# Kernel optimization log

Hardware: AMD Instinct MI355X
Metric: run time of the kernel (lower is better)

## Reference

```python
import jax, jax.numpy as jnp
import numpy as np

B, T, H = 4, 2048, 1024
NH = 16
HD = H // NH  # 64
NEG_INF = -1.0e9  # module uses -1e9, not -inf


def setup_inputs() -> dict:
    key = jax.random.key(0)
    k1, k2, k3 = jax.random.split(key, 3)
    x = jax.random.normal(k1, (B, T, H), dtype=jnp.float32)
    W_qkv = jax.random.normal(k2, (3 * H, H), dtype=jnp.float32) * (1.0 / np.sqrt(H))
    W_out = jax.random.normal(k3, (H, H), dtype=jnp.float32) * (1.0 / np.sqrt(H))
    return {"x": x, "W_qkv": W_qkv, "W_out": W_out}


def reference(x, W_qkv, W_out):
    Bx, Tx, C = x.shape
    qkv = x @ W_qkv.T                              # [B,T,3H]
    q, k, v = jnp.split(qkv, 3, axis=-1)
    # [B,T,H] -> [B,NH,T,HD]
    q = q.reshape(Bx, Tx, NH, HD).transpose(0, 2, 1, 3)
    k = k.reshape(Bx, Tx, NH, HD).transpose(0, 2, 1, 3)
    v = v.reshape(Bx, Tx, NH, HD).transpose(0, 2, 1, 3)
    scale = 1.0 / np.sqrt(HD)
    scores = jnp.einsum('bhqd,bhkd->bhqk', q, k) * scale  # [B,NH,T,T]
    causal = jnp.tril(jnp.ones((Tx, Tx), dtype=bool))[None, None]
    scores = jnp.where(causal, scores, jnp.asarray(NEG_INF, scores.dtype))
    attn = jax.nn.softmax(scores, axis=-1)
    out = jnp.einsum('bhqk,bhkd->bhqd', attn, v)   # [B,NH,T,HD]
    out = out.transpose(0, 2, 1, 3).reshape(Bx, Tx, C)
    return out @ W_out.T
```

## Files before the change

### kernel.cpp

```cpp
#include <hip/hip_runtime.h>
#include <hip/hip_bf16.h>


typedef unsigned short ushort_t;
typedef __attribute__((ext_vector_type(8))) short  s8v;
typedef __attribute__((ext_vector_type(4))) float  f4v;
typedef __attribute__((ext_vector_type(4))) unsigned int u4v;

__device__ inline ushort_t f2bf(float f) {
    unsigned u = __builtin_bit_cast(unsigned, f);
    u += 0x7fffu + ((u >> 16) & 1u);
    return (ushort_t)(u >> 16);
}

__device__ inline void gload16(const ushort_t* g, ushort_t* l) {
    __builtin_amdgcn_global_load_lds(
        (const __attribute__((address_space(1))) unsigned int*)g,
        (__attribute__((address_space(3))) unsigned int*)l, 16, 0, 0);
}

__global__ __launch_bounds__(256) void cast_all(
    const float* __restrict__ x, const float* __restrict__ wqkv,
    const float* __restrict__ wout, ushort_t* __restrict__ xb,
    ushort_t* __restrict__ wqkvb, ushort_t* __restrict__ woutb)
{
    int i = blockIdx.x * 256 + threadIdx.x;
    const float* src; ushort_t* dst; int off;
    if (i < 1048576)      { src = x;    dst = xb;    off = i; }
    else if (i < 1441792) { src = wqkv; dst = wqkvb; off = i - 1048576; }
    else                  { src = wout; dst = woutb; off = i - 1441792; }
    const float* p = src + (size_t)off * 8;
    f4v a = *(const f4v*)p;
    f4v b = *(const f4v*)(p + 4);
    union { u4v v; ushort_t u[8]; } o;
    #pragma unroll
    for (int j = 0; j < 4; j++) { o.u[j] = f2bf(a[j]); o.u[j + 4] = f2bf(b[j]); }
    *(u4v*)(dst + (size_t)off * 8) = o.v;
}

template<int MODE>
__global__ __launch_bounds__(256) void gemm_nt(
    const ushort_t* __restrict__ A, const ushort_t* __restrict__ Bm,
    ushort_t* __restrict__ o0, ushort_t* __restrict__ o1, ushort_t* __restrict__ o2,
    float* __restrict__ of)
{
    __shared__ __align__(16) ushort_t SH[32768];

    const int tid  = threadIdx.x;
    const int m0   = blockIdx.x * 128;
    const int n0   = blockIdx.y * 128;
    const int wave = tid >> 6, lane = tid & 63;
    const int wr = wave >> 1, wc = wave & 1;
    const int lhi = lane >> 4, llo = lane & 15;
    const int sgch = ((lane & 7) ^ (lane >> 3)) * 8;

    auto stage = [&](int k0, int buf) {
        #pragma unroll
        for (int p = 0; p < 4; p++) {
            int row = wave * 32 + p * 8 + (lane >> 3);
            gload16(A  + (size_t)(m0 + row) * 1024 + k0 + sgch,
                    &SH[buf * 8192 + row * 64 + (lane & 7) * 8]);
            gload16(Bm + (size_t)(n0 + row) * 1024 + k0 + sgch,
                    &SH[16384 + buf * 8192 + row * 64 + (lane & 7) * 8]);
        }
    };

    f4v acc[4][4] = {};
    int buf = 0;
    const int xs = llo & 7;

    stage(0, 0);
    __syncthreads();

    for (int k0 = 0; k0 < 1024; k0 += 64) {
        if (k0 + 64 < 1024) stage(k0 + 64, buf ^ 1);

        #pragma unroll
        for (int s = 0; s < 2; s++) {
            s8v a[4], b[4];
            #pragma unroll
            for (int i = 0; i < 4; i++)
                a[i] = *(const s8v*)&SH[buf * 8192
                        + (wr * 64 + i * 16 + llo) * 64 + ((s * 4 + lhi) ^ xs) * 8];
            #pragma unroll
            for (int i = 0; i < 4; i++)
                b[i] = *(const s8v*)&SH[16384 + buf * 8192
                        + (wc * 64 + i * 16 + llo) * 64 + ((s * 4 + lhi) ^ xs) * 8];
            #pragma unroll
            for (int i = 0; i < 4; i++)
                #pragma unroll
                for (int j = 0; j < 4; j++)
                    acc[i][j] = __builtin_amdgcn_mfma_f32_16x16x32_bf16(a[i], b[j], acc[i][j], 0, 0, 0);
        }

        __syncthreads();
        buf ^= 1;
    }

    if (MODE == 0 && n0 >= 2048) {
        const int hbase = (n0 - 2048) >> 6;
        const int t0b   = m0 & 2047;
        const int bb    = m0 >> 11;
        #pragma unroll 1
        for (int p = 0; p < 2; p++) {
            __syncthreads();
            if (wr == p) {
                #pragma unroll
                for (int i = 0; i < 4; i++)
                    #pragma unroll
                    for (int j = 0; j < 4; j++) {
                        union { unsigned long long q; ushort_t u[4]; } w;
                        #pragma unroll
                        for (int r = 0; r < 4; r++) w.u[r] = f2bf(acc[i][j][r]);
                        int nrel = wc * 64 + j * 16 + llo;
                        *(unsigned long long*)&SH[nrel * 68 + i * 16 + lhi * 4] = w.q;
                    }
            }
            __syncthreads();
            #pragma unroll
            for (int cc = 0; cc < 4; cc++) {
                int c  = cc * 256 + tid;
                int nn = c >> 3, sp0 = (c & 7) * 8;
                union { s8v v; ushort_t u[8]; } o;
                #pragma unroll
                for (int i2 = 0; i2 < 8; i2++) {
                    int sp = sp0 + i2;
                    int k  = ((sp >> 5) << 5) | ((sp & 1) << 4) | ((sp & 31) >> 1);
                    o.u[i2] = SH[nn * 68 + k];
                }
                int head = hbase + (nn >> 6), d = nn & 63;
                size_t bh = (size_t)(bb * 16 + head);
                *(s8v*)(o2 + ((bh * 64 + d) * 2048 + t0b + p * 64 + sp0)) = o.v;
            }
        }
        return;
    }

    #pragma unroll
    for (int i = 0; i < 4; i++) {
        #pragma unroll
        for (int j = 0; j < 4; j++) {
            #pragma unroll
            for (int r = 0; r < 4; r++) {
                int m = m0 + wr * 64 + i * 16 + lhi * 4 + r;
                int n = n0 + wc * 64 + j * 16 + llo;
                if (MODE == 1) {
                    of[(size_t)m * 1024 + n] = acc[i][j][r];
                } else {
                    float val = acc[i][j][r];
                    int b  = m >> 11, t = m & 2047;
                    int which = n >> 10, hh = n & 1023;
                    int head = hh >> 6, d = hh & 63;
                    size_t bh = (size_t)(b * 16 + head);
                    if (which == 0)
                        o0[(size_t)m * 1024 + hh] = f2bf(val * 0.18033688011112042f);
                    else
                        o1[(bh * 2048 + t) * 64 + d] = f2bf(val);
                }
            }
        }
    }
}

__global__ __launch_bounds__(512, 4) void attn_kernel(
    const ushort_t* __restrict__ q_ws, const ushort_t* __restrict__ k_ws,
    const ushort_t* __restrict__ v_ws, ushort_t* __restrict__ ao_ws)
{
    const int bh   = blockIdx.y;
    const int p    = (bh < 32) ? blockIdx.x : 7 - blockIdx.x;
    const int tid  = threadIdx.x;
    const int wave = tid >> 6, lane = tid & 63;
    const int lhi = lane >> 4, llo = lane & 15;
    const int b = bh >> 4, head = bh & 15;

    const ushort_t* Kb = k_ws + (size_t)bh * 2048 * 64;
    const ushort_t* Vb = v_ws + (size_t)bh * 64 * 2048;

    __shared__ __align__(16) ushort_t Ks [2][4096];
    __shared__ __align__(16) ushort_t Vts[2][4096];
    __shared__ __align__(16) ushort_t Ps [8][2][1280];

    const int srow = wave * 8 + (lane >> 3);
    const int gch  = ((lane & 7) ^ (srow & 7)) * 8;
    auto stage = [&](int t, int buf) {
        const int kk0 = t * 64;
        gload16(Kb + (size_t)(kk0 + srow) * 64 + gch,
                &Ks[buf][srow * 64 + (lane & 7) * 8]);
        gload16(Vb + (size_t)srow * 2048 + kk0 + gch,
                &Vts[buf][srow * 64 + (lane & 7) * 8]);
    };

    const int qt  = (wave >> 2) ? (15 - p) : p;
    const int wq0 = qt * 128 + (wave & 3) * 32;

    s8v qf[2][2];
    #pragma unroll
    for (int g = 0; g < 2; g++) {
        const ushort_t* Qp = q_ws + (size_t)(b * 2048 + wq0 + g * 16 + llo) * 1024 + head * 64;
        qf[g][0] = *(const s8v*)(Qp + lhi * 8);
        qf[g][1] = *(const s8v*)(Qp + 32 + lhi * 8);
    }

    f4v o[2][4] = {};
    float lsum[2][4] = {};

    const int ntb = 32 - 2 * p;
    const int xs  = llo & 7;
    int cur = 0;

    stage(0, 0);
    __syncthreads();

    #pragma unroll 1
    for (int t = 0; t < ntb; t++) {
        if (t + 1 < ntb) stage(t + 1, cur ^ 1);

        const int kk0 = t * 64;
        if (kk0 <= wq0 + 31) {
            f4v s0[4], s1[4];
            __builtin_amdgcn_s_setprio(1);
            #pragma unroll
            for (int c = 0; c < 4; c++) {
                const int rb = (c * 16 + llo) * 64;
                s8v kb0 = *(const s8v*)&Ks[cur][rb + ((lhi    ) ^ xs) * 8];
                s8v kb1 = *(const s8v*)&Ks[cur][rb + ((4 + lhi) ^ xs) * 8];
                f4v z0 = {}, z1 = {};
                z0 = __builtin_amdgcn_mfma_f32_16x16x32_bf16(qf[0][0], kb0, z0, 0, 0, 0);
                z0 = __builtin_amdgcn_mfma_f32_16x16x32_bf16(qf[0][1], kb1, z0, 0, 0, 0);
                z1 = __builtin_amdgcn_mfma_f32_16x16x32_bf16(qf[1][0], kb0, z1, 0, 0, 0);
                z1 = __builtin_amdgcn_mfma_f32_16x16x32_bf16(qf[1][1], kb1, z1, 0, 0, 0);
                s0[c] = z0; s1[c] = z1;
            }
            __builtin_amdgcn_s_setprio(0);

            #pragma unroll
            for (int g = 0; g < 2; g++) {
                const int qrb = wq0 + g * 16;
                f4v* s = g ? s1 : s0;
                if ((kk0 + 63) > qrb) {
                    #pragma unroll
                    for (int c = 0; c < 4; c++) {
                        int kkg = kk0 + c * 16 + llo;
                        #pragma unroll
                        for (int r = 0; r < 4; r++)
                            if (kkg > qrb + lhi * 4 + r) s[c][r] = -1e9f;
                    }
                }
                #pragma unroll
                for (int h = 0; h < 2; h++) {
                    #pragma unroll
                    for (int r = 0; r < 4; r++) {
                        float p0 = __builtin_amdgcn_exp2f(s[2 * h][r]);
                        float p1 = __builtin_amdgcn_exp2f(s[2 * h + 1][r]);
                        lsum[g][r] += p0 + p1;
                        unsigned pk;
                        asm("v_cvt_pk_bf16_f32 %0, %1, %2" : "=v"(pk) : "v"(p0), "v"(p1));
                        *(unsigned*)&Ps[wave][g][h * 640 + (lhi * 4 + r) * 40 + llo * 2] = pk;
                    }
                }
            }

            s8v pa[2][2];
            #pragma unroll
            for (int g = 0; g < 2; g++) {
                pa[g][0] = *(const s8v*)&Ps[wave][g][llo * 40 + lhi * 8];
                pa[g][1] = *(const s8v*)&Ps[wave][g][640 + llo * 40 + lhi * 8];
            }
            __builtin_amdgcn_s_setprio(1);
            #pragma unroll
            for (int cd = 0; cd < 4; cd++) {
                const int rb = (cd * 16 + llo) * 64;
                s8v vb0 = *(const s8v*)&Vts[cur][rb + ((lhi    ) ^ xs) * 8];
                s8v vb1 = *(const s8v*)&Vts[cur][rb + ((4 + lhi) ^ xs) * 8];
                #pragma unroll
                for (int g = 0; g < 2; g++) {
                    o[g][cd] = __builtin_amdgcn_mfma_f32_16x16x32_bf16(pa[g][0], vb0, o[g][cd], 0, 0, 0);
                    o[g][cd] = __builtin_amdgcn_mfma_f32_16x16x32_bf16(pa[g][1], vb1, o[g][cd], 0, 0, 0);
                }
            }
            __builtin_amdgcn_s_setprio(0);
        }

        __syncthreads();
        cur ^= 1;
    }

    #pragma unroll
    for (int off = 1; off < 16; off <<= 1)
        #pragma unroll
        for (int g = 0; g < 2; g++)
            #pragma unroll
            for (int r = 0; r < 4; r++)
                lsum[g][r] += __shfl_xor(lsum[g][r], off, 64);

    #pragma unroll
    for (int g = 0; g < 2; g++)
        #pragma unroll
        for (int cd = 0; cd < 4; cd++)
            #pragma unroll
            for (int r = 0; r < 4; r++) {
                int qq = wq0 + g * 16 + lhi * 4 + r;
                int d  = cd * 16 + llo;
                ao_ws[((size_t)(b * 2048 + qq)) * 1024 + head * 64 + d] =
                    f2bf(o[g][cd][r] / lsum[g][r]);
            }
}

extern "C" void kernel_launch(void* const* d_in, const int* in_sizes, int n_in,
                              void* d_out, int out_size, void* d_ws, size_t ws_size,
                              hipStream_t stream) {
    const float* x    = (const float*)d_in[0];
    const float* wqkv = (const float*)d_in[1];
    const float* wout = (const float*)d_in[2];

    ushort_t* wqkvb = (ushort_t*)d_ws;
    ushort_t* woutb = wqkvb + 3145728;
    ushort_t* xb    = woutb + 1048576;
    ushort_t* q_ws  = xb + 8388608;
    ushort_t* k_ws  = q_ws + 8388608;
    ushort_t* v_ws  = k_ws + 8388608;
    ushort_t* ao_ws = xb;
    float*    out   = (float*)d_out;

    cast_all<<<6144, 256, 0, stream>>>(x, wqkv, wout, xb, wqkvb, woutb);
    gemm_nt<0><<<dim3(64, 24), 256, 0, stream>>>(xb, wqkvb, q_ws, k_ws, v_ws, nullptr);
    attn_kernel<<<dim3(8, 64), 512, 0, stream>>>(q_ws, k_ws, v_ws, ao_ws);
    gemm_nt<1><<<dim3(64, 8), 256, 0, stream>>>(ao_ws, woutb, nullptr, nullptr, nullptr, out);
}
```

Before: 225.5 us.

## Give each attention wave 64 query rows with 4 waves per block

Attention blocks shrink from 8 waves to 4, and each wave now covers 64 query rows (four 16-row groups) instead of 32. K and V fragments loaded from LDS are reused across four MFMA row groups, which cuts LDS reads per unit of compute. Diagonal masking now applies only to the single tile where the key block equals the wave's query start, and each wave loads two staging chunks per tile. The cost is more accumulator registers and lower occupancy (launch bound of 256 threads, 2 blocks per CU), so there is less latency hiding.

```diff
diff --git a/kernel.cpp b/kernel.cpp
--- a/kernel.cpp
+++ b/kernel.cpp
@@ -162,7 +162,7 @@
     }
 }
 
-__global__ __launch_bounds__(512, 4) void attn_kernel(
+__global__ __launch_bounds__(256, 2) void attn_kernel(
     const ushort_t* __restrict__ q_ws, const ushort_t* __restrict__ k_ws,
     const ushort_t* __restrict__ v_ws, ushort_t* __restrict__ ao_ws)
 {
@@ -178,31 +178,34 @@
 
     __shared__ __align__(16) ushort_t Ks [2][4096];
     __shared__ __align__(16) ushort_t Vts[2][4096];
-    __shared__ __align__(16) ushort_t Ps [8][2][1280];
-
-    const int srow = wave * 8 + (lane >> 3);
-    const int gch  = ((lane & 7) ^ (srow & 7)) * 8;
+    __shared__ __align__(16) ushort_t Ps [4][4][1280];
+
+    const int gch = ((lane & 7) ^ (lane >> 3)) * 8;
     auto stage = [&](int t, int buf) {
         const int kk0 = t * 64;
-        gload16(Kb + (size_t)(kk0 + srow) * 64 + gch,
-                &Ks[buf][srow * 64 + (lane & 7) * 8]);
-        gload16(Vb + (size_t)srow * 2048 + kk0 + gch,
-                &Vts[buf][srow * 64 + (lane & 7) * 8]);
+        #pragma unroll
+        for (int i = 0; i < 2; i++) {
+            int row = wave * 8 + 32 * i + (lane >> 3);
+            gload16(Kb + (size_t)(kk0 + row) * 64 + gch,
+                    &Ks[buf][(wave * 64 + 256 * i + lane) * 8]);
+            gload16(Vb + (size_t)row * 2048 + kk0 + gch,
+                    &Vts[buf][(wave * 64 + 256 * i + lane) * 8]);
+        }
     };
 
-    const int qt  = (wave >> 2) ? (15 - p) : p;
-    const int wq0 = qt * 128 + (wave & 3) * 32;
-
-    s8v qf[2][2];
-    #pragma unroll
-    for (int g = 0; g < 2; g++) {
+    const int qt  = (wave >> 1) ? (15 - p) : p;
+    const int wq0 = qt * 128 + (wave & 1) * 64;
+
+    s8v qf[4][2];
+    #pragma unroll
+    for (int g = 0; g < 4; g++) {
         const ushort_t* Qp = q_ws + (size_t)(b * 2048 + wq0 + g * 16 + llo) * 1024 + head * 64;
         qf[g][0] = *(const s8v*)(Qp + lhi * 8);
         qf[g][1] = *(const s8v*)(Qp + 32 + lhi * 8);
     }
 
-    f4v o[2][4] = {};
-    float lsum[2][4] = {};
+    f4v o[4][4] = {};
+    float lsum[4][4] = {};
 
     const int ntb = 32 - 2 * p;
     const int xs  = llo & 7;
@@ -216,28 +219,31 @@
         if (t + 1 < ntb) stage(t + 1, cur ^ 1);
 
         const int kk0 = t * 64;
-        if (kk0 <= wq0 + 31) {
-            f4v s0[4], s1[4];
-            __builtin_amdgcn_s_setprio(1);
+        if (kk0 <= wq0) {
+            const bool dm = (kk0 == wq0);
+
+            s8v kb[4][2];
             #pragma unroll
             for (int c = 0; c < 4; c++) {
                 const int rb = (c * 16 + llo) * 64;
-                s8v kb0 = *(const s8v*)&Ks[cur][rb + ((lhi    ) ^ xs) * 8];
-                s8v kb1 = *(const s8v*)&Ks[cur][rb + ((4 + lhi) ^ xs) * 8];
-                f4v z0 = {}, z1 = {};
-                z0 = __builtin_amdgcn_mfma_f32_16x16x32_bf16(qf[0][0], kb0, z0, 0, 0, 0);
-                z0 = __builtin_amdgcn_mfma_f32_16x16x32_bf16(qf[0][1], kb1, z0, 0, 0, 0);
-                z1 = __builtin_amdgcn_mfma_f32_16x16x32_bf16(qf[1][0], kb0, z1, 0, 0, 0);
-                z1 = __builtin_amdgcn_mfma_f32_16x16x32_bf16(qf[1][1], kb1, z1, 0, 0, 0);
-                s0[c] = z0; s1[c] = z1;
-            }
-            __builtin_amdgcn_s_setprio(0);
-
-            #pragma unroll
-            for (int g = 0; g < 2; g++) {
+                kb[c][0] = *(const s8v*)&Ks[cur][rb + ((lhi    ) ^ xs) * 8];
+                kb[c][1] = *(const s8v*)&Ks[cur][rb + ((4 + lhi) ^ xs) * 8];
+            }
+
+            #pragma unroll
+            for (int g = 0; g < 4; g++) {
                 const int qrb = wq0 + g * 16;
-                f4v* s = g ? s1 : s0;
-                if ((kk0 + 63) > qrb) {
+                f4v s[4];
+                __builtin_amdgcn_s_setprio(1);
+                #pragma unroll
+                for (int c = 0; c < 4; c++) {
+                    f4v z = {};
+                    z = __builtin_amdgcn_mfma_f32_16x16x32_bf16(qf[g][0], kb[c][0], z, 0, 0, 0);
+                    z = __builtin_amdgcn_mfma_f32_16x16x32_bf16(qf[g][1], kb[c][1], z, 0, 0, 0);
+                    s[c] = z;
+                }
+                __builtin_amdgcn_s_setprio(0);
+                if (dm) {
                     #pragma unroll
                     for (int c = 0; c < 4; c++) {
                         int kkg = kk0 + c * 16 + llo;
@@ -260,25 +266,25 @@
                 }
             }
 
-            s8v pa[2][2];
-            #pragma unroll
-            for (int g = 0; g < 2; g++) {
-                pa[g][0] = *(const s8v*)&Ps[wave][g][llo * 40 + lhi * 8];
-                pa[g][1] = *(const s8v*)&Ps[wave][g][640 + llo * 40 + lhi * 8];
-            }
-            __builtin_amdgcn_s_setprio(1);
+            s8v vb[4][2];
             #pragma unroll
             for (int cd = 0; cd < 4; cd++) {
                 const int rb = (cd * 16 + llo) * 64;
-                s8v vb0 = *(const s8v*)&Vts[cur][rb + ((lhi    ) ^ xs) * 8];
-                s8v vb1 = *(const s8v*)&Vts[cur][rb + ((4 + lhi) ^ xs) * 8];
-                #pragma unroll
-                for (int g = 0; g < 2; g++) {
-                    o[g][cd] = __builtin_amdgcn_mfma_f32_16x16x32_bf16(pa[g][0], vb0, o[g][cd], 0, 0, 0);
-                    o[g][cd] = __builtin_amdgcn_mfma_f32_16x16x32_bf16(pa[g][1], vb1, o[g][cd], 0, 0, 0);
-                }
-            }
-            __builtin_amdgcn_s_setprio(0);
+                vb[cd][0] = *(const s8v*)&Vts[cur][rb + ((lhi    ) ^ xs) * 8];
+                vb[cd][1] = *(const s8v*)&Vts[cur][rb + ((4 + lhi) ^ xs) * 8];
+            }
+            #pragma unroll
+            for (int g = 0; g < 4; g++) {
+                s8v pa0 = *(const s8v*)&Ps[wave][g][llo * 40 + lhi * 8];
+                s8v pa1 = *(const s8v*)&Ps[wave][g][640 + llo * 40 + lhi * 8];
+                __builtin_amdgcn_s_setprio(1);
+                #pragma unroll
+                for (int cd = 0; cd < 4; cd++) {
+                    o[g][cd] = __builtin_amdgcn_mfma_f32_16x16x32_bf16(pa0, vb[cd][0], o[g][cd], 0, 0, 0);
+                    o[g][cd] = __builtin_amdgcn_mfma_f32_16x16x32_bf16(pa1, vb[cd][1], o[g][cd], 0, 0, 0);
+                }
+                __builtin_amdgcn_s_setprio(0);
+            }
         }
 
         __syncthreads();
@@ -288,13 +294,13 @@
     #pragma unroll
     for (int off = 1; off < 16; off <<= 1)
         #pragma unroll
-        for (int g = 0; g < 2; g++)
+        for (int g = 0; g < 4; g++)
             #pragma unroll
             for (int r = 0; r < 4; r++)
                 lsum[g][r] += __shfl_xor(lsum[g][r], off, 64);
 
     #pragma unroll
-    for (int g = 0; g < 2; g++)
+    for (int g = 0; g < 4; g++)
         #pragma unroll
         for (int cd = 0; cd < 4; cd++)
             #pragma unroll
@@ -324,6 +330,6 @@
 
     cast_all<<<6144, 256, 0, stream>>>(x, wqkv, wout, xb, wqkvb, woutb);
     gemm_nt<0><<<dim3(64, 24), 256, 0, stream>>>(xb, wqkvb, q_ws, k_ws, v_ws, nullptr);
-    attn_kernel<<<dim3(8, 64), 512, 0, stream>>>(q_ws, k_ws, v_ws, ao_ws);
+    attn_kernel<<<dim3(8, 64), 256, 0, stream>>>(q_ws, k_ws, v_ws, ao_ws);
     gemm_nt<1><<<dim3(64, 8), 256, 0, stream>>>(ao_ws, woutb, nullptr, nullptr, nullptr, out);
 }
```

New measurement: 243.3 us. +7.9%, slower.

## Split attention work across 16 waves with 16 query rows each

Applied to the files above, without the earlier changes.

Doubles the attention block to 1024 threads so each wave handles 16 query rows instead of 32. K staging is split onto the first half of the waves and V staging onto the second half. The intent is more waves in flight to hide latency and finer causal skipping per wave. In exchange, each K/V tile is reused by fewer rows per wave, barriers cover more waves, and register pressure per wave changes under the new launch bounds.

```diff
diff --git a/kernel.cpp b/kernel.cpp
--- a/kernel.cpp
+++ b/kernel.cpp
@@ -162,7 +162,7 @@
     }
 }
 
-__global__ __launch_bounds__(512, 4) void attn_kernel(
+__global__ __launch_bounds__(1024, 8) void attn_kernel(
     const ushort_t* __restrict__ q_ws, const ushort_t* __restrict__ k_ws,
     const ushort_t* __restrict__ v_ws, ushort_t* __restrict__ ao_ws)
 {
@@ -170,6 +170,7 @@
     const int p    = (bh < 32) ? blockIdx.x : 7 - blockIdx.x;
     const int tid  = threadIdx.x;
     const int wave = tid >> 6, lane = tid & 63;
+    const int half = wave >> 3, wsub = wave & 7;
     const int lhi = lane >> 4, llo = lane & 15;
     const int b = bh >> 4, head = bh & 15;
 
@@ -178,31 +179,32 @@
 
     __shared__ __align__(16) ushort_t Ks [2][4096];
     __shared__ __align__(16) ushort_t Vts[2][4096];
-    __shared__ __align__(16) ushort_t Ps [8][2][1280];
-
-    const int srow = wave * 8 + (lane >> 3);
-    const int gch  = ((lane & 7) ^ (srow & 7)) * 8;
+    __shared__ __align__(16) ushort_t Ps [16][1280];
+
+    const int gch = ((lane & 7) ^ (lane >> 3)) * 8;
     auto stage = [&](int t, int buf) {
         const int kk0 = t * 64;
-        gload16(Kb + (size_t)(kk0 + srow) * 64 + gch,
-                &Ks[buf][srow * 64 + (lane & 7) * 8]);
-        gload16(Vb + (size_t)srow * 2048 + kk0 + gch,
-                &Vts[buf][srow * 64 + (lane & 7) * 8]);
+        const int row = wsub * 8 + (lane >> 3);
+        if (half == 0)
+            gload16(Kb + (size_t)(kk0 + row) * 64 + gch,
+                    &Ks[buf][(wsub * 64 + lane) * 8]);
+        else
+            gload16(Vb + (size_t)row * 2048 + kk0 + gch,
+                    &Vts[buf][(wsub * 64 + lane) * 8]);
     };
 
-    const int qt  = (wave >> 2) ? (15 - p) : p;
-    const int wq0 = qt * 128 + (wave & 3) * 32;
-
-    s8v qf[2][2];
-    #pragma unroll
-    for (int g = 0; g < 2; g++) {
-        const ushort_t* Qp = q_ws + (size_t)(b * 2048 + wq0 + g * 16 + llo) * 1024 + head * 64;
-        qf[g][0] = *(const s8v*)(Qp + lhi * 8);
-        qf[g][1] = *(const s8v*)(Qp + 32 + lhi * 8);
-    }
-
-    f4v o[2][4] = {};
-    float lsum[2][4] = {};
+    const int qt  = half ? (15 - p) : p;
+    const int wq0 = qt * 128 + wsub * 16;
+
+    s8v qf0, qf1;
+    {
+        const ushort_t* Qp = q_ws + (size_t)(b * 2048 + wq0 + llo) * 1024 + head * 64;
+        qf0 = *(const s8v*)(Qp + lhi * 8);
+        qf1 = *(const s8v*)(Qp + 32 + lhi * 8);
+    }
+
+    f4v o[4] = {};
+    float lsum[4] = {};
 
     const int ntb = 32 - 2 * p;
     const int xs  = llo & 7;
@@ -216,67 +218,53 @@
         if (t + 1 < ntb) stage(t + 1, cur ^ 1);
 
         const int kk0 = t * 64;
-        if (kk0 <= wq0 + 31) {
-            f4v s0[4], s1[4];
+        if (kk0 <= wq0 + 15) {
+            f4v s[4];
             __builtin_amdgcn_s_setprio(1);
             #pragma unroll
             for (int c = 0; c < 4; c++) {
                 const int rb = (c * 16 + llo) * 64;
                 s8v kb0 = *(const s8v*)&Ks[cur][rb + ((lhi    ) ^ xs) * 8];
                 s8v kb1 = *(const s8v*)&Ks[cur][rb + ((4 + lhi) ^ xs) * 8];
-                f4v z0 = {}, z1 = {};
-                z0 = __builtin_amdgcn_mfma_f32_16x16x32_bf16(qf[0][0], kb0, z0, 0, 0, 0);
-                z0 = __builtin_amdgcn_mfma_f32_16x16x32_bf16(qf[0][1], kb1, z0, 0, 0, 0);
-                z1 = __builtin_amdgcn_mfma_f32_16x16x32_bf16(qf[1][0], kb0, z1, 0, 0, 0);
-                z1 = __builtin_amdgcn_mfma_f32_16x16x32_bf16(qf[1][1], kb1, z1, 0, 0, 0);
-                s0[c] = z0; s1[c] = z1;
+                f4v z = {};
+                z = __builtin_amdgcn_mfma_f32_16x16x32_bf16(qf0, kb0, z, 0, 0, 0);
+                z = __builtin_amdgcn_mfma_f32_16x16x32_bf16(qf1, kb1, z, 0, 0, 0);
+                s[c] = z;
             }
             __builtin_amdgcn_s_setprio(0);
 
-            #pragma unroll
-            for (int g = 0; g < 2; g++) {
-                const int qrb = wq0 + g * 16;
-                f4v* s = g ? s1 : s0;
-                if ((kk0 + 63) > qrb) {
+            if (kk0 + 63 > wq0) {
+                #pragma unroll
+                for (int c = 0; c < 4; c++) {
+                    int kkg = kk0 + c * 16 + llo;
                     #pragma unroll
-                    for (int c = 0; c < 4; c++) {
-                        int kkg = kk0 + c * 16 + llo;
-                        #pragma unroll
-                        for (int r = 0; r < 4; r++)
-                            if (kkg > qrb + lhi * 4 + r) s[c][r] = -1e9f;
-                    }
+                    for (int r = 0; r < 4; r++)
+                        if (kkg > wq0 + lhi * 4 + r) s[c][r] = -1e9f;
                 }
-                #pragma unroll
-                for (int h = 0; h < 2; h++) {
-                    #pragma unroll
-                    for (int r = 0; r < 4; r++) {
-                        float p0 = __builtin_amdgcn_exp2f(s[2 * h][r]);
-                        float p1 = __builtin_amdgcn_exp2f(s[2 * h + 1][r]);
-                        lsum[g][r] += p0 + p1;
-                        unsigned pk;
-                        asm("v_cvt_pk_bf16_f32 %0, %1, %2" : "=v"(pk) : "v"(p0), "v"(p1));
-                        *(unsigned*)&Ps[wave][g][h * 640 + (lhi * 4 + r) * 40 + llo * 2] = pk;
-                    }
+            }
+            #pragma unroll
+            for (int h = 0; h < 2; h++) {
+                #pragma unroll
+                for (int r = 0; r < 4; r++) {
+                    float p0 = __builtin_amdgcn_exp2f(s[2 * h][r]);
+                    float p1 = __builtin_amdgcn_exp2f(s[2 * h + 1][r]);
+                    lsum[r] += p0 + p1;
+                    unsigned pk;
+                    asm("v_cvt_pk_bf16_f32 %0, %1, %2" : "=v"(pk) : "v"(p0), "v"(p1));
+                    *(unsigned*)&Ps[wave][h * 640 + (lhi * 4 + r) * 40 + llo * 2] = pk;
                 }
             }
 
-            s8v pa[2][2];
-            #pragma unroll
-            for (int g = 0; g < 2; g++) {
-                pa[g][0] = *(const s8v*)&Ps[wave][g][llo * 40 + lhi * 8];
-                pa[g][1] = *(const s8v*)&Ps[wave][g][640 + llo * 40 + lhi * 8];
-            }
+            s8v pa0 = *(const s8v*)&Ps[wave][llo * 40 + lhi * 8];
+            s8v pa1 = *(const s8v*)&Ps[wave][640 + llo * 40 + lhi * 8];
             __builtin_amdgcn_s_setprio(1);
             #pragma unroll
             for (int cd = 0; cd < 4; cd++) {
                 const int rb = (cd * 16 + llo) * 64;
                 s8v vb0 = *(const s8v*)&Vts[cur][rb + ((lhi    ) ^ xs) * 8];
                 s8v vb1 = *(const s8v*)&Vts[cur][rb + ((4 + lhi) ^ xs) * 8];
-                #pragma unroll
-                for (int g = 0; g < 2; g++) {
-                    o[g][cd] = __builtin_amdgcn_mfma_f32_16x16x32_bf16(pa[g][0], vb0, o[g][cd], 0, 0, 0);
-                    o[g][cd] = __builtin_amdgcn_mfma_f32_16x16x32_bf16(pa[g][1], vb1, o[g][cd], 0, 0, 0);
-                }
+                o[cd] = __builtin_amdgcn_mfma_f32_16x16x32_bf16(pa0, vb0, o[cd], 0, 0, 0);
+                o[cd] = __builtin_amdgcn_mfma_f32_16x16x32_bf16(pa1, vb1, o[cd], 0, 0, 0);
             }
             __builtin_amdgcn_s_setprio(0);
         }
@@ -288,22 +276,18 @@
     #pragma unroll
     for (int off = 1; off < 16; off <<= 1)
         #pragma unroll
-        for (int g = 0; g < 2; g++)
-            #pragma unroll
-            for (int r = 0; r < 4; r++)
-                lsum[g][r] += __shfl_xor(lsum[g][r], off, 64);
+        for (int r = 0; r < 4; r++)
+            lsum[r] += __shfl_xor(lsum[r], off, 64);
 
     #pragma unroll
-    for (int g = 0; g < 2; g++)
-        #pragma unroll
-        for (int cd = 0; cd < 4; cd++)
-            #pragma unroll
-            for (int r = 0; r < 4; r++) {
-                int qq = wq0 + g * 16 + lhi * 4 + r;
-                int d  = cd * 16 + llo;
-                ao_ws[((size_t)(b * 2048 + qq)) * 1024 + head * 64 + d] =
-                    f2bf(o[g][cd][r] / lsum[g][r]);
-            }
+    for (int cd = 0; cd < 4; cd++)
+        #pragma unroll
+        for (int r = 0; r < 4; r++) {
+            int qq = wq0 + lhi * 4 + r;
+            int d  = cd * 16 + llo;
+            ao_ws[((size_t)(b * 2048 + qq)) * 1024 + head * 64 + d] =
+                f2bf(o[cd][r] / lsum[r]);
+        }
 }
 
 extern "C" void kernel_launch(void* const* d_in, const int* in_sizes, int n_in,
@@ -324,6 +308,6 @@
 
     cast_all<<<6144, 256, 0, stream>>>(x, wqkv, wout, xb, wqkvb, woutb);
     gemm_nt<0><<<dim3(64, 24), 256, 0, stream>>>(xb, wqkvb, q_ws, k_ws, v_ws, nullptr);
-    attn_kernel<<<dim3(8, 64), 512, 0, stream>>>(q_ws, k_ws, v_ws, ao_ws);
+    attn_kernel<<<dim3(8, 64), 1024, 0, stream>>>(q_ws, k_ws, v_ws, ao_ws);
     gemm_nt<1><<<dim3(64, 8), 256, 0, stream>>>(ao_ws, woutb, nullptr, nullptr, nullptr, out);
 }
```

Result: no change. 227.2 us (+0.8%).
